# Kernel tuning notes

Hardware: AMD Instinct MI355X
Metric: run time of the kernel (lower is better)

The kernel has to match this reference:

```python
import jax, jax.numpy as jnp
import numpy as np

N = 50000       # num_nodes
E = 1_600_000   # num_edges (avg degree 32)
F_IN, HID, F_OUT = 128, 128, 64


def setup_inputs() -> dict:
    key = jax.random.key(0)
    k0, k1, k2, k3 = jax.random.split(key, 4)
    x = jax.random.normal(k0, (1, N, F_IN), dtype=jnp.float32)
    edge_index = jax.random.randint(k1, (2, E), 0, N, dtype=jnp.int32)
    # GCNConv weights (glorot-ish scale) and zero biases
    W1 = jax.random.normal(k2, (F_IN, HID), dtype=jnp.float32) / np.float32(np.sqrt(F_IN))
    b1 = jnp.zeros((HID,), dtype=jnp.float32)
    W2 = jax.random.normal(k3, (HID, F_OUT), dtype=jnp.float32) / np.float32(np.sqrt(HID))
    b2 = jnp.zeros((F_OUT,), dtype=jnp.float32)
    return {"x": x, "edge_index": edge_index, "W1": W1, "b1": b1, "W2": W2, "b2": b2}


def _gcn_layer(h, src, dst, norm, W, b, n):
    # linear transform then symmetric-normalized scatter-add aggregation
    h = h @ W                              # [N, F_out]
    msg = h[src] * norm[:, None]           # [E+N, F_out] gathered messages
    agg = jax.ops.segment_sum(msg, dst, num_segments=n)
    return agg + b


def reference(x, edge_index, W1, b1, W2, b2):
    xn = x[0]                              # [N, F_in] node feature matrix
    n = xn.shape[0]
    src, dst = edge_index[0], edge_index[1]
    # add self-loops (GCNConv default)
    loops = jnp.arange(n, dtype=src.dtype)
    src = jnp.concatenate([src, loops])
    dst = jnp.concatenate([dst, loops])
    # symmetric normalization: deg^-1/2[src] * deg^-1/2[dst] (deg >= 1 w/ self-loops)
    deg = jax.ops.segment_sum(jnp.ones(dst.shape, dtype=xn.dtype), dst, num_segments=n)
    dinv = jax.lax.rsqrt(deg)
    norm = dinv[src] * dinv[dst]
    h = jax.nn.relu(_gcn_layer(xn, src, dst, norm, W1, b1, n))
    out = jax.nn.relu(_gcn_layer(h, src, dst, norm, W2, b2, n))
    return out
```

## Files before the change

kernel.cpp:

```cpp
#include <hip/hip_runtime.h>
#include <hip/hip_fp16.h>


#define TILE 8192
#define BIN_CAP 2560

typedef _Float16 half8 __attribute__((ext_vector_type(8)));
typedef float floatx4 __attribute__((ext_vector_type(4)));

__global__ __launch_bounds__(512) void bin_kernel(const int* __restrict__ src,
                                                  const int* __restrict__ dst, int E,
                                                  int nbins,
                                                  int* __restrict__ binCnt,
                                                  unsigned* __restrict__ recs) {
    extern __shared__ int lds[];
    int* cnt = lds;
    int* gbase = lds + nbins;
    int tid = threadIdx.x;
    for (int i = tid; i < nbins; i += 512) cnt[i] = 0;
    __syncthreads();

    int t0 = blockIdx.x * TILE;
    int tEnd = min(t0 + TILE, E);

    for (int e = t0 + tid; e < tEnd; e += 512)
        atomicAdd(&cnt[dst[e] >> 6], 1);
    __syncthreads();

    for (int i = tid; i < nbins; i += 512) {
        int c = cnt[i];
        gbase[i] = (c > 0) ? atomicAdd(&binCnt[i], c) : 0;
        cnt[i] = 0;
    }
    __syncthreads();

    for (int e = t0 + tid; e < tEnd; e += 512) {
        int d = dst[e];
        int s = src[e];
        int b = d >> 6;
        int r = atomicAdd(&cnt[b], 1);
        int g = gbase[b] + r;
        if (g < BIN_CAP)
            recs[(size_t)b * BIN_CAP + g] = ((unsigned)(d & 63) << 16) | (unsigned)s;
    }
}

__global__ __launch_bounds__(512) void sort_bins(const unsigned* __restrict__ recs,
                                                 const int* __restrict__ binCnt,
                                                 unsigned short* __restrict__ sortedG,
                                                 int* __restrict__ startG,
                                                 float* __restrict__ dinv, int N) {
    __shared__ unsigned short sorted[BIN_CAP];
    __shared__ int c64[64];
    __shared__ int start[65];
    __shared__ int cursor[64];
    int b = blockIdx.x, tid = threadIdx.x;
    int lane = tid & 63, wave = tid >> 6;

    if (tid < 64) c64[tid] = 0;
    __syncthreads();
    int cnt = min(binCnt[b], BIN_CAP);
    const unsigned* bin = recs + (size_t)b * BIN_CAP;

    for (int i = tid; i < cnt; i += 512)
        atomicAdd(&c64[bin[i] >> 16], 1);
    __syncthreads();

    if (wave == 0) {
        int c = c64[lane];
        int v = c;
        #pragma unroll
        for (int off = 1; off < 64; off <<= 1) {
            int t = __shfl_up(v, off);
            if (lane >= off) v += t;
        }
        start[lane] = v - c;
        cursor[lane] = v - c;
        startG[b * 65 + lane] = v - c;
        if (lane == 63) { start[64] = v; startG[b * 65 + 64] = v; }
        int n = (b << 6) + lane;
        if (n < N) dinv[n] = rsqrtf((float)(c + 1));
    }
    __syncthreads();

    for (int i = tid; i < cnt; i += 512) {
        unsigned r = bin[i];
        int pos = atomicAdd(&cursor[r >> 16], 1);
        sorted[pos] = (unsigned short)(r & 0xFFFFu);
    }
    __syncthreads();
    unsigned short* sg = sortedG + (size_t)b * BIN_CAP;
    for (int i = tid; i < cnt; i += 512) sg[i] = sorted[i];
}

template <int COLS, bool FP32IN>
__global__ __launch_bounds__(256) void gemm_mfma(const void* __restrict__ Xv,
                                                 const float* __restrict__ W,
                                                 const float* __restrict__ dinv,
                                                 __half* __restrict__ Y, int N) {
    constexpr int LDA = 136;
    __shared__ __align__(16) _Float16 aT[64 * LDA];
    __shared__ __align__(16) _Float16 bT[COLS * LDA];

    int tid = threadIdx.x;
    int lane = tid & 63, wave = tid >> 6;
    int row0 = blockIdx.x * 64;

    for (int i = tid * 4; i < 64 * 128; i += 1024) {
        int r = i >> 7, k = i & 127;
        int gr = row0 + r;
        if (FP32IN) {
            float4 v = make_float4(0.f, 0.f, 0.f, 0.f);
            if (gr < N) v = *(const float4*)&((const float*)Xv)[(size_t)gr * 128 + k];
            __half2 p0 = __floats2half2_rn(v.x, v.y);
            __half2 p1 = __floats2half2_rn(v.z, v.w);
            *(uint2*)&aT[r * LDA + k] = make_uint2(*(uint*)&p0, *(uint*)&p1);
        } else {
            ushort4 u = make_ushort4(0, 0, 0, 0);
            if (gr < N) u = *(const ushort4*)&((const __half*)Xv)[(size_t)gr * 128 + k];
            *(ushort4*)&aT[r * LDA + k] = u;
        }
    }
    for (int i = tid; i < 128 * COLS; i += 256) {
        int k = i / COLS, n = i % COLS;
        bT[n * LDA + k] = (_Float16)W[i];
    }
    __syncthreads();

    constexpr int NT = COLS / 16;
    floatx4 acc[NT];
    #pragma unroll
    for (int t = 0; t < NT; t++) acc[t] = (floatx4){0.f, 0.f, 0.f, 0.f};

    int m = lane & 15, q = lane >> 4;
    const _Float16* arow = &aT[(wave * 16 + m) * LDA + q * 8];

    #pragma unroll
    for (int ks = 0; ks < 4; ks++) {
        half8 af = *(const half8*)&arow[ks * 32];
        #pragma unroll
        for (int t = 0; t < NT; t++) {
            half8 bf = *(const half8*)&bT[(t * 16 + m) * LDA + ks * 32 + q * 8];
            acc[t] = __builtin_amdgcn_mfma_f32_16x16x32_f16(af, bf, acc[t], 0, 0, 0);
        }
    }
    __syncthreads();

    float dv[4];
    #pragma unroll
    for (int r = 0; r < 4; r++) {
        int gr = row0 + wave * 16 + q * 4 + r;
        dv[r] = (gr < N) ? dinv[gr] : 0.0f;
    }
    #pragma unroll
    for (int t = 0; t < NT; t++)
        #pragma unroll
        for (int r = 0; r < 4; r++)
            aT[(wave * 16 + q * 4 + r) * LDA + t * 16 + m] = (_Float16)(dv[r] * acc[t][r]);
    __syncthreads();

    for (int i = tid; i < 64 * (COLS / 2); i += 256) {
        int r = i / (COLS / 2), c = i % (COLS / 2);
        int gr = row0 + r;
        if (gr < N)
            ((uint*)Y)[(size_t)gr * (COLS / 2) + c] = *(uint*)&aT[r * LDA + c * 2];
    }
}

__global__ __launch_bounds__(512) void agg_128(const __half* __restrict__ G,
                                               const unsigned short* __restrict__ sortedG,
                                               const int* __restrict__ startG,
                                               const float* __restrict__ dinv,
                                               const float* __restrict__ bias,
                                               __half* __restrict__ out, int N) {
    __shared__ unsigned short buf[BIN_CAP];
    __shared__ int st[33];
    int b = blockIdx.x, half_ = blockIdx.y;
    int tid = threadIdx.x, lane = tid & 63, wave = tid >> 6;
    int ql = lane & 15, quad = lane >> 4;
    int r0 = half_ * 32;

    if (tid < 33) st[tid] = startG[b * 65 + r0 + tid];
    __syncthreads();
    int S0 = st[0], S1 = st[32];
    const unsigned short* sg = sortedG + (size_t)b * BIN_CAP;
    for (int i = tid; i < S1 - S0; i += 512) buf[i] = sg[S0 + i];
    __syncthreads();

    float bb[8];
    #pragma unroll
    for (int k = 0; k < 4; k++) {
        float2 t = *(const float2*)&bias[ql * 8 + k * 2];
        bb[k * 2] = t.x; bb[k * 2 + 1] = t.y;
    }

    for (int rr = 0; rr < 4; rr++) {
        int row = wave * 4 + rr;
        int n = (b << 6) + r0 + row;
        if (n >= N) continue;
        int jst = st[row] - S0, jen = st[row + 1] - S0;

        float ax[8] = {};
        int j = jst + quad;
        for (; j + 4 < jen; j += 8) {
            int sA = buf[j], sB = buf[j + 4];
            uint4 uA = *(const uint4*)&G[(size_t)sA * 128 + ql * 8];
            uint4 uB = *(const uint4*)&G[(size_t)sB * 128 + ql * 8];
            float2 f;
            f = __half22float2(*(__half2*)&uA.x); ax[0] += f.x; ax[1] += f.y;
            f = __half22float2(*(__half2*)&uA.y); ax[2] += f.x; ax[3] += f.y;
            f = __half22float2(*(__half2*)&uA.z); ax[4] += f.x; ax[5] += f.y;
            f = __half22float2(*(__half2*)&uA.w); ax[6] += f.x; ax[7] += f.y;
            f = __half22float2(*(__half2*)&uB.x); ax[0] += f.x; ax[1] += f.y;
            f = __half22float2(*(__half2*)&uB.y); ax[2] += f.x; ax[3] += f.y;
            f = __half22float2(*(__half2*)&uB.z); ax[4] += f.x; ax[5] += f.y;
            f = __half22float2(*(__half2*)&uB.w); ax[6] += f.x; ax[7] += f.y;
        }
        for (; j < jen; j += 4) {
            int s = buf[j];
            uint4 u = *(const uint4*)&G[(size_t)s * 128 + ql * 8];
            float2 f;
            f = __half22float2(*(__half2*)&u.x); ax[0] += f.x; ax[1] += f.y;
            f = __half22float2(*(__half2*)&u.y); ax[2] += f.x; ax[3] += f.y;
            f = __half22float2(*(__half2*)&u.z); ax[4] += f.x; ax[5] += f.y;
            f = __half22float2(*(__half2*)&u.w); ax[6] += f.x; ax[7] += f.y;
        }
        #pragma unroll
        for (int k = 0; k < 8; k++) {
            ax[k] += __shfl_xor(ax[k], 16);
            ax[k] += __shfl_xor(ax[k], 32);
        }
        if (quad == 0) {
            uint4 us = *(const uint4*)&G[(size_t)n * 128 + ql * 8];
            float2 f;
            f = __half22float2(*(__half2*)&us.x); ax[0] += f.x; ax[1] += f.y;
            f = __half22float2(*(__half2*)&us.y); ax[2] += f.x; ax[3] += f.y;
            f = __half22float2(*(__half2*)&us.z); ax[4] += f.x; ax[5] += f.y;
            f = __half22float2(*(__half2*)&us.w); ax[6] += f.x; ax[7] += f.y;
            float di = dinv[n];
            __half2 h[4];
            #pragma unroll
            for (int k = 0; k < 4; k++) {
                float o0 = fmaxf(fmaf(di, ax[k * 2],     bb[k * 2]),     0.0f);
                float o1 = fmaxf(fmaf(di, ax[k * 2 + 1], bb[k * 2 + 1]), 0.0f);
                h[k] = __floats2half2_rn(o0, o1);
            }
            *(uint4*)&out[(size_t)n * 128 + ql * 8] = *(uint4*)h;
        }
    }
}

__global__ __launch_bounds__(512) void agg_64(const __half* __restrict__ G,
                                              const unsigned short* __restrict__ sortedG,
                                              const int* __restrict__ startG,
                                              const float* __restrict__ dinv,
                                              const float* __restrict__ bias,
                                              float* __restrict__ out, int N) {
    __shared__ unsigned short buf[BIN_CAP];
    __shared__ int st[33];
    int b = blockIdx.x, half_ = blockIdx.y;
    int tid = threadIdx.x, lane = tid & 63, wave = tid >> 6;
    int ol = lane & 7, oct = lane >> 3;
    int r0 = half_ * 32;

    if (tid < 33) st[tid] = startG[b * 65 + r0 + tid];
    __syncthreads();
    int S0 = st[0], S1 = st[32];
    const unsigned short* sg = sortedG + (size_t)b * BIN_CAP;
    for (int i = tid; i < S1 - S0; i += 512) buf[i] = sg[S0 + i];
    __syncthreads();

    float bb[8];
    #pragma unroll
    for (int k = 0; k < 4; k++) {
        float2 t = *(const float2*)&bias[ol * 8 + k * 2];
        bb[k * 2] = t.x; bb[k * 2 + 1] = t.y;
    }

    for (int rr = 0; rr < 4; rr++) {
        int row = wave * 4 + rr;
        int n = (b << 6) + r0 + row;
        if (n >= N) continue;
        int jst = st[row] - S0, jen = st[row + 1] - S0;

        float ax[8] = {};
        int j = jst + oct;
        for (; j + 8 < jen; j += 16) {
            int sA = buf[j], sB = buf[j + 8];
            uint4 uA = *(const uint4*)&G[(size_t)sA * 64 + ol * 8];
            uint4 uB = *(const uint4*)&G[(size_t)sB * 64 + ol * 8];
            float2 f;
            f = __half22float2(*(__half2*)&uA.x); ax[0] += f.x; ax[1] += f.y;
            f = __half22float2(*(__half2*)&uA.y); ax[2] += f.x; ax[3] += f.y;
            f = __half22float2(*(__half2*)&uA.z); ax[4] += f.x; ax[5] += f.y;
            f = __half22float2(*(__half2*)&uA.w); ax[6] += f.x; ax[7] += f.y;
            f = __half22float2(*(__half2*)&uB.x); ax[0] += f.x; ax[1] += f.y;
            f = __half22float2(*(__half2*)&uB.y); ax[2] += f.x; ax[3] += f.y;
            f = __half22float2(*(__half2*)&uB.z); ax[4] += f.x; ax[5] += f.y;
            f = __half22float2(*(__half2*)&uB.w); ax[6] += f.x; ax[7] += f.y;
        }
        for (; j < jen; j += 8) {
            int s = buf[j];
            uint4 u = *(const uint4*)&G[(size_t)s * 64 + ol * 8];
            float2 f;
            f = __half22float2(*(__half2*)&u.x); ax[0] += f.x; ax[1] += f.y;
            f = __half22float2(*(__half2*)&u.y); ax[2] += f.x; ax[3] += f.y;
            f = __half22float2(*(__half2*)&u.z); ax[4] += f.x; ax[5] += f.y;
            f = __half22float2(*(__half2*)&u.w); ax[6] += f.x; ax[7] += f.y;
        }
        #pragma unroll
        for (int k = 0; k < 8; k++) {
            ax[k] += __shfl_xor(ax[k], 8);
            ax[k] += __shfl_xor(ax[k], 16);
            ax[k] += __shfl_xor(ax[k], 32);
        }
        if (oct < 2) {
            uint4 us = *(const uint4*)&G[(size_t)n * 64 + ol * 8];
            float2 f;
            f = __half22float2(*(__half2*)&us.x); ax[0] += f.x; ax[1] += f.y;
            f = __half22float2(*(__half2*)&us.y); ax[2] += f.x; ax[3] += f.y;
            f = __half22float2(*(__half2*)&us.z); ax[4] += f.x; ax[5] += f.y;
            f = __half22float2(*(__half2*)&us.w); ax[6] += f.x; ax[7] += f.y;
            float di = dinv[n];
            float o[8];
            #pragma unroll
            for (int k = 0; k < 8; k++)
                o[k] = fmaxf(fmaf(di, ax[k], bb[k]), 0.0f);
            if (oct == 0)
                *(float4*)&out[(size_t)n * 64 + ol * 8] = make_float4(o[0], o[1], o[2], o[3]);
            else
                *(float4*)&out[(size_t)n * 64 + ol * 8 + 4] = make_float4(o[4], o[5], o[6], o[7]);
        }
    }
}

extern "C" void kernel_launch(void* const* d_in, const int* in_sizes, int n_in,
                              void* d_out, int out_size, void* d_ws, size_t ws_size,
                              hipStream_t stream) {
    const float* x  = (const float*)d_in[0];
    const int*   ei = (const int*)d_in[1];
    const float* W1 = (const float*)d_in[2];
    const float* b1 = (const float*)d_in[3];
    const float* W2 = (const float*)d_in[4];
    const float* b2 = (const float*)d_in[5];
    float* out = (float*)d_out;

    const int HID  = in_sizes[3];
    const int F_IN = in_sizes[2] / HID;
    const int N    = in_sizes[0] / F_IN;
    const int E    = in_sizes[1] / 2;
    (void)n_in; (void)out_size; (void)ws_size; (void)F_IN;

    const int* src = ei;
    const int* dst = ei + E;

    const int nbins = (N + 63) >> 6;

    char* p = (char*)d_ws;
    auto carve = [&](size_t bytes) { void* q = (void*)p; p += (bytes + 255) & ~(size_t)255; return q; };
    int*            binCnt  = (int*)           carve((size_t)nbins * 4);
    float*          dinv    = (float*)         carve((size_t)N * 4);
    unsigned*       recs    = (unsigned*)      carve((size_t)nbins * BIN_CAP * 4);
    unsigned short* sortedG = (unsigned short*)carve((size_t)nbins * BIN_CAP * 2);
    int*            startG  = (int*)           carve((size_t)nbins * 65 * 4);
    __half*         bufG    = (__half*)        carve((size_t)N * 128 * 2);
    __half*         bufB    = (__half*)        carve((size_t)N * 128 * 2);

    hipMemsetAsync(binCnt, 0, (size_t)nbins * 4, stream);

    int numTiles = (E + TILE - 1) / TILE;
    size_t binLds = (size_t)nbins * 2 * 4;
    bin_kernel<<<numTiles, 512, binLds, stream>>>(src, dst, E, nbins, binCnt, recs);
    sort_bins<<<nbins, 512, 0, stream>>>(recs, binCnt, sortedG, startG, dinv, N);

    dim3 aggGrid(nbins, 2);
    int gemmGrid = (N + 63) / 64;

    gemm_mfma<128, true><<<gemmGrid, 256, 0, stream>>>(x, W1, dinv, bufG, N);
    agg_128<<<aggGrid, 512, 0, stream>>>(bufG, sortedG, startG, dinv, b1, bufB, N);

    gemm_mfma<64, false><<<gemmGrid, 256, 0, stream>>>(bufB, W2, dinv, bufG, N);
    agg_64<<<aggGrid, 512, 0, stream>>>(bufG, sortedG, startG, dinv, b2, out, N);
}
```

Measured before the change: 218.2 us.

## Fuse first-layer aggregation with second-layer GEMM in one kernel

Merges agg_128 and the second gemm_mfma into a single kernel. Each block aggregates 64 rows into LDS, then multiplies them by W2 with MFMA and writes the 64-wide fp16 output directly. This removes one launch and the round trip of the N×128 intermediate through global memory. In exchange each block now handles 64 rows instead of 32, so there are half as many blocks, and each block reconverts W2 into LDS, which raises LDS use and lowers parallelism.

New measurement: 213.5 us. 2.2% less time.

```diff
diff --git a/kernel.cpp b/kernel.cpp
--- a/kernel.cpp
+++ b/kernel.cpp
@@ -167,24 +167,33 @@
     }
 }
 
-__global__ __launch_bounds__(512) void agg_128(const __half* __restrict__ G,
-                                               const unsigned short* __restrict__ sortedG,
-                                               const int* __restrict__ startG,
-                                               const float* __restrict__ dinv,
-                                               const float* __restrict__ bias,
-                                               __half* __restrict__ out, int N) {
+__global__ __launch_bounds__(512) void agg_gemm_fused(
+        const __half* __restrict__ G,
+        const unsigned short* __restrict__ sortedG,
+        const int* __restrict__ startG,
+        const float* __restrict__ dinv,
+        const float* __restrict__ bias,
+        const float* __restrict__ W2,
+        __half* __restrict__ Y2, int N) {
+    constexpr int LDH = 136;
     __shared__ unsigned short buf[BIN_CAP];
-    __shared__ int st[33];
-    int b = blockIdx.x, half_ = blockIdx.y;
+    __shared__ int st[65];
+    __shared__ __align__(16) _Float16 hT[64 * LDH];
+    __shared__ __align__(16) _Float16 bT[64 * LDH];
+
+    int b = blockIdx.x;
     int tid = threadIdx.x, lane = tid & 63, wave = tid >> 6;
     int ql = lane & 15, quad = lane >> 4;
-    int r0 = half_ * 32;
-
-    if (tid < 33) st[tid] = startG[b * 65 + r0 + tid];
-    __syncthreads();
-    int S0 = st[0], S1 = st[32];
+
+    if (tid < 65) st[tid] = startG[b * 65 + tid];
+    __syncthreads();
+    int cnt = st[64];
     const unsigned short* sg = sortedG + (size_t)b * BIN_CAP;
-    for (int i = tid; i < S1 - S0; i += 512) buf[i] = sg[S0 + i];
+    for (int i = tid; i < cnt; i += 512) buf[i] = sg[i];
+    for (int i = tid; i < 128 * 64; i += 512) {
+        int k = i >> 6, n = i & 63;
+        bT[n * LDH + k] = (_Float16)W2[i];
+    }
     __syncthreads();
 
     float bb[8];
@@ -194,11 +203,17 @@
         bb[k * 2] = t.x; bb[k * 2 + 1] = t.y;
     }
 
-    for (int rr = 0; rr < 4; rr++) {
-        int row = wave * 4 + rr;
-        int n = (b << 6) + r0 + row;
-        if (n >= N) continue;
-        int jst = st[row] - S0, jen = st[row + 1] - S0;
+    for (int rr = 0; rr < 8; rr++) {
+        int row = wave * 8 + rr;
+        int n = (b << 6) + row;
+        if (n >= N) {
+            if (quad == 0) {
+                uint4 z = make_uint4(0, 0, 0, 0);
+                *(uint4*)&hT[row * LDH + ql * 8] = z;
+            }
+            continue;
+        }
+        int jst = st[row], jen = st[row + 1];
 
         float ax[8] = {};
         int j = jst + quad;
@@ -245,8 +260,44 @@
                 float o1 = fmaxf(fmaf(di, ax[k * 2 + 1], bb[k * 2 + 1]), 0.0f);
                 h[k] = __floats2half2_rn(o0, o1);
             }
-            *(uint4*)&out[(size_t)n * 128 + ql * 8] = *(uint4*)h;
-        }
+            *(uint4*)&hT[row * LDH + ql * 8] = *(uint4*)h;
+        }
+    }
+    __syncthreads();
+
+    int m = lane & 15, q = lane >> 4;
+    int mt = wave & 3, nt0 = (wave >> 2) * 2;
+    floatx4 acc[2] = {(floatx4){0.f, 0.f, 0.f, 0.f}, (floatx4){0.f, 0.f, 0.f, 0.f}};
+    const _Float16* arow = &hT[(mt * 16 + m) * LDH + q * 8];
+    #pragma unroll
+    for (int ks = 0; ks < 4; ks++) {
+        half8 af = *(const half8*)&arow[ks * 32];
+        #pragma unroll
+        for (int t = 0; t < 2; t++) {
+            half8 bf = *(const half8*)&bT[((nt0 + t) * 16 + m) * LDH + ks * 32 + q * 8];
+            acc[t] = __builtin_amdgcn_mfma_f32_16x16x32_f16(af, bf, acc[t], 0, 0, 0);
+        }
+    }
+    __syncthreads();
+
+    float dv[4];
+    #pragma unroll
+    for (int r = 0; r < 4; r++) {
+        int gr = (b << 6) + mt * 16 + q * 4 + r;
+        dv[r] = (gr < N) ? dinv[gr] : 0.0f;
+    }
+    #pragma unroll
+    for (int t = 0; t < 2; t++)
+        #pragma unroll
+        for (int r = 0; r < 4; r++)
+            hT[(mt * 16 + q * 4 + r) * LDH + (nt0 + t) * 16 + m] = (_Float16)(dv[r] * acc[t][r]);
+    __syncthreads();
+
+    for (int i = tid; i < 64 * 32; i += 512) {
+        int r = i >> 5, c = i & 31;
+        int gr = (b << 6) + r;
+        if (gr < N)
+            ((uint*)Y2)[(size_t)gr * 32 + c] = *(uint*)&hT[r * LDH + c * 2];
     }
 }
 
@@ -364,7 +415,7 @@
     unsigned short* sortedG = (unsigned short*)carve((size_t)nbins * BIN_CAP * 2);
     int*            startG  = (int*)           carve((size_t)nbins * 65 * 4);
     __half*         bufG    = (__half*)        carve((size_t)N * 128 * 2);
-    __half*         bufB    = (__half*)        carve((size_t)N * 128 * 2);
+    __half*         bufG2   = (__half*)        carve((size_t)N * 64 * 2);
 
     hipMemsetAsync(binCnt, 0, (size_t)nbins * 4, stream);
 
@@ -373,12 +424,12 @@
     bin_kernel<<<numTiles, 512, binLds, stream>>>(src, dst, E, nbins, binCnt, recs);
     sort_bins<<<nbins, 512, 0, stream>>>(recs, binCnt, sortedG, startG, dinv, N);
 
+    int gemmGrid = (N + 63) / 64;
+
+    gemm_mfma<128, true><<<gemmGrid, 256, 0, stream>>>(x, W1, dinv, bufG, N);
+
+    agg_gemm_fused<<<nbins, 512, 0, stream>>>(bufG, sortedG, startG, dinv, b1, W2, bufG2, N);
+
     dim3 aggGrid(nbins, 2);
-    int gemmGrid = (N + 63) / 64;
-
-    gemm_mfma<128, true><<<gemmGrid, 256, 0, stream>>>(x, W1, dinv, bufG, N);
-    agg_128<<<aggGrid, 512, 0, stream>>>(bufG, sortedG, startG, dinv, b1, bufB, N);
-
-    gemm_mfma<64, false><<<gemmGrid, 256, 0, stream>>>(bufB, W2, dinv, bufG, N);
-    agg_64<<<aggGrid, 512, 0, stream>>>(bufG, sortedG, startG, dinv, b2, out, N);
-}
+    agg_64<<<aggGrid, 512, 0, stream>>>(bufG2, sortedG, startG, dinv, b2, out, N);
+}
```
